# Kernel optimization log

Measured on AMD Instinct MI355X. Metric: run time of the kernel, lower is better.

Reference implementation:

```python
import jax, jax.numpy as jnp
import numpy as np

DIM = 768
NUM_HEADS = 12
HEAD_DIM = DIM // NUM_HEADS
SCALE = HEAD_DIM ** -0.5


def setup_inputs() -> dict:
    key = jax.random.key(0)
    ks = jax.random.split(key, 5)
    B, N, C = 2, 2048, DIM
    x = jax.random.normal(ks[0], (B, N, C), dtype=jnp.float32)
    # Dense layers: kernel [in, out], bias [out]
    w_qkv = jax.random.normal(ks[1], (C, 3 * C), dtype=jnp.float32) * (1.0 / np.sqrt(C))
    b_qkv = jnp.zeros((3 * C,), dtype=jnp.float32)
    w_proj = jax.random.normal(ks[2], (C, C), dtype=jnp.float32) * (1.0 / np.sqrt(C))
    b_proj = jnp.zeros((C,), dtype=jnp.float32)
    return {"x": x, "w_qkv": w_qkv, "b_qkv": b_qkv, "w_proj": w_proj, "b_proj": b_proj}


def reference(x, w_qkv, b_qkv, w_proj, b_proj):
    B, N, C = x.shape
    H, D = NUM_HEADS, HEAD_DIM
    qkv = x @ w_qkv + b_qkv                      # [B, N, 3C]
    qkv = qkv.reshape(B, N, 3, H, D).transpose(2, 0, 3, 1, 4)  # [3, B, H, N, D]
    q, k, v = qkv[0], qkv[1], qkv[2]
    # NOTE: original code applies scale AFTER q@k^T (scales scores), same math
    attn = jnp.einsum("bhnd,bhmd->bhnm", q, k) * SCALE  # [B, H, N, N]
    attn = jax.nn.softmax(attn, axis=-1)
    out = jnp.einsum("bhnm,bhmd->bhnd", attn, v)        # [B, H, N, D]
    out = out.transpose(0, 2, 1, 3).reshape(B, N, C)
    return out @ w_proj + b_proj
```

## Files before the change

kernel.cpp:

```cpp
#include <hip/hip_runtime.h>
#include <stdint.h>

typedef unsigned short u16;

typedef __bf16 bf16x8_ __attribute__((ext_vector_type(8)));
typedef float f32x4 __attribute__((ext_vector_type(4)));
typedef float f32x4__ __attribute__((ext_vector_type(4)));
typedef unsigned int u32x4_ __attribute__((ext_vector_type(4)));
typedef unsigned int u32x2_ __attribute__((ext_vector_type(2)));

typedef bf16x8_ __attribute__((may_alias)) bf16x8;
typedef u32x4_ __attribute__((may_alias)) u32x4;
typedef u32x2_ __attribute__((may_alias)) u32x2;
typedef f32x4__ __attribute__((may_alias)) f32x4a;

#define MFMA16(a, b, c) __builtin_amdgcn_mfma_f32_16x16x32_bf16(a, b, c, 0, 0, 0)
#define EXP2(x) __builtin_amdgcn_exp2f(x)

#define BN 2048
#define CDIM 768
#define HEADS 12
#define HD 64
#define NBH 24
#define MROWS 4096
#define QSC 0.1803368801111244f
#define SMAX 16.0f

__device__ __forceinline__ u16 f2bf(float f) {
    __bf16 h = (__bf16)f;
    return __builtin_bit_cast(u16, h);
}

__device__ __forceinline__ void gload_lds16(const void* g, void* l) {
    auto* gp = reinterpret_cast<const __attribute__((address_space(1))) unsigned int*>(
        reinterpret_cast<uintptr_t>(g));
    auto* lp = reinterpret_cast<__attribute__((address_space(3))) unsigned int*>(
        reinterpret_cast<uintptr_t>(l));
    __builtin_amdgcn_global_load_lds(gp, lp, 16, 0, 0);
}

__global__ void cast_x_kernel(const float* __restrict__ in, u16* __restrict__ out, int n8) {
    int i = blockIdx.x * 256 + threadIdx.x;
    if (i >= n8) return;
    const f32x4a* p = (const f32x4a*)in;
    f32x4a a = p[2 * (size_t)i], b = p[2 * (size_t)i + 1];
    union { u16 h[8]; u32x4_ v; } o;
#pragma unroll
    for (int j = 0; j < 4; ++j) { o.h[j] = f2bf(a[j]); o.h[4 + j] = f2bf(b[j]); }
    *(u32x4*)(out + (size_t)8 * i) = o.v;
}

__global__ void transpose_to_bf16(const float* __restrict__ in, u16* __restrict__ out,
                                  int R, int C) {
    __shared__ u16 tile[64][66];
    int r0 = blockIdx.y * 64, c0 = blockIdx.x * 64;
    int tid = threadIdx.x;
#pragma unroll
    for (int i = 0; i < 16; ++i) {
        int idx = tid + i * 256;
        int r = idx >> 6, c = idx & 63;
        tile[r][c] = f2bf(in[(size_t)(r0 + r) * C + c0 + c]);
    }
    __syncthreads();
#pragma unroll
    for (int i = 0; i < 16; ++i) {
        int idx = tid + i * 256;
        int c = idx >> 6, r = idx & 63;
        out[(size_t)(c0 + c) * R + r0 + r] = tile[r][c];
    }
}

__global__ void transpose_v(const u16* __restrict__ in, u16* __restrict__ out) {
    __shared__ u16 tile[64][66];
    int bh = blockIdx.z, r0 = blockIdx.y * 64;
    const u16* pin = in + (size_t)bh * BN * HD;
    u16* pout = out + (size_t)bh * HD * BN;
    int tid = threadIdx.x;
#pragma unroll
    for (int i = 0; i < 2; ++i) {
        int idx = tid + i * 256;
        int r = idx >> 3, ch = idx & 7;
        u32x4 v = *(const u32x4*)(pin + (size_t)(r0 + r) * HD + ch * 8);
        *(u32x4*)(&tile[r][ch * 8]) = v;
    }
    __syncthreads();
#pragma unroll
    for (int i = 0; i < 16; ++i) {
        int idx = tid + i * 256;
        int c = idx >> 6, r = idx & 63;
        pout[(size_t)c * BN + r0 + r] = tile[r][c];
    }
}

template <int EPI>
__global__ __launch_bounds__(256) void gemm_bt(
    const u16* __restrict__ A, const u16* __restrict__ Bt,
    const float* __restrict__ bias, int M, int N, int K,
    u16* __restrict__ Qb, u16* __restrict__ Kb, u16* __restrict__ Vb,
    float* __restrict__ Out) {
    __shared__ u16 As[2][128 * 64];
    __shared__ u16 Bs[2][128 * 64];
    int tid = threadIdx.x;
    int wid = tid >> 6, lane = tid & 63, lr = lane & 15, lhi = lane >> 4;
    int wr = wid >> 1, wc = wid & 1;
    int m0 = blockIdx.x * 128, n0 = blockIdx.y * 128;

    int rsub = lane >> 3;
    int csw = ((lane & 7) ^ rsub) * 8;

    auto stage = [&](int b, int k0) {
#pragma unroll
        for (int it = 0; it < 4; ++it) {
            int grp = it * 4 + wid;
            int row = grp * 8 + rsub;
            gload_lds16(A + (size_t)(m0 + row) * K + k0 + csw, &As[b][grp * 512]);
            gload_lds16(Bt + (size_t)(n0 + row) * K + k0 + csw, &Bs[b][grp * 512]);
        }
    };

    f32x4 acc[4][4];
#pragma unroll
    for (int i = 0; i < 4; ++i)
#pragma unroll
        for (int j = 0; j < 4; ++j) acc[i][j] = f32x4{0.f, 0.f, 0.f, 0.f};

    stage(0, 0);
    __syncthreads();
    int cur = 0;

    for (int k0 = 0; k0 < K; k0 += 64) {
        if (k0 + 64 < K) stage(cur ^ 1, k0 + 64);

        const u16* Ac = As[cur];
        const u16* Bc = Bs[cur];
        bf16x8 af[2][4], bfr[2][4];
#pragma unroll
        for (int x = 0; x < 4; ++x) {
            int ra = wr * 64 + x * 16 + lr;
            af[0][x] = *(const bf16x8*)(Ac + ra * 64 + ((lhi ^ (ra & 7)) * 8));
            af[1][x] = *(const bf16x8*)(Ac + ra * 64 + (((4 + lhi) ^ (ra & 7)) * 8));
            int rb = wc * 64 + x * 16 + lr;
            bfr[0][x] = *(const bf16x8*)(Bc + rb * 64 + ((lhi ^ (rb & 7)) * 8));
            bfr[1][x] = *(const bf16x8*)(Bc + rb * 64 + (((4 + lhi) ^ (rb & 7)) * 8));
        }
#pragma unroll
        for (int kc = 0; kc < 2; ++kc)
#pragma unroll
            for (int mi = 0; mi < 4; ++mi)
#pragma unroll
                for (int ni = 0; ni < 4; ++ni)
                    acc[mi][ni] = MFMA16(af[kc][mi], bfr[kc][ni], acc[mi][ni]);

        __syncthreads();
        cur ^= 1;
    }

#pragma unroll
    for (int mi = 0; mi < 4; ++mi) {
#pragma unroll
        for (int ni = 0; ni < 4; ++ni) {
            int col = n0 + wc * 64 + ni * 16 + lr;
            float bv = bias[col];
#pragma unroll
            for (int j = 0; j < 4; ++j) {
                int row = m0 + wr * 64 + mi * 16 + lhi * 4 + j;
                float v = acc[mi][ni][j] + bv;
                if constexpr (EPI == 0) {
                    int three = (col >= 1536) ? 2 : (col >= 768 ? 1 : 0);
                    int rem = col - three * 768;
                    int h = rem >> 6, d = rem & 63;
                    int b = row >> 11, nn = row & 2047;
                    size_t dst = ((size_t)(b * HEADS + h) * BN + nn) * HD + d;
                    if (three == 0)      Qb[dst] = f2bf(v * QSC);
                    else if (three == 1) Kb[dst] = f2bf(v);
                    else                 Vb[dst] = f2bf(v);
                } else {
                    Out[(size_t)row * N + col] = v;
                }
            }
        }
    }
}

__global__ __launch_bounds__(256) void attn_kernel(
    const u16* __restrict__ Qb, const u16* __restrict__ Kb,
    const u16* __restrict__ Vt, u16* __restrict__ Ao) {
    __shared__ u16 Ks[2][64 * 64];
    __shared__ u16 Vs[2][64 * 64];
    __shared__ u16 Ps[4][16 * 64];
    int tid = threadIdx.x, wid = tid >> 6, lane = tid & 63, lr = lane & 15, lhi = lane >> 4;
    int bh = blockIdx.y;
    int q0 = blockIdx.x * 64;

    const u16* Kbase = Kb + (size_t)bh * BN * HD;
    const u16* Vbase = Vt + (size_t)bh * HD * BN;
    int srow = lane >> 3;
    int csw = ((lane & 7) ^ srow) * 8;

    auto stageKV = [&](int b, int tn) {
#pragma unroll
        for (int it = 0; it < 2; ++it) {
            int r0 = it * 32 + wid * 8;
            gload_lds16(Kbase + (size_t)(tn + r0 + srow) * HD + csw, &Ks[b][r0 * 64]);
            gload_lds16(Vbase + (size_t)(r0 + srow) * BN + tn + csw, &Vs[b][r0 * 64]);
        }
    };

    const u16* Qrow = Qb + ((size_t)bh * BN + q0 + wid * 16 + lr) * HD;
    bf16x8 qf0 = *(const bf16x8*)(Qrow + lhi * 8);
    bf16x8 qf1 = *(const bf16x8*)(Qrow + 32 + lhi * 8);

    f32x4 po[4];
#pragma unroll
    for (int i = 0; i < 4; ++i) po[i] = f32x4{0.f, 0.f, 0.f, 0.f};
    float lrun = 0.f;
    u16* Pw = Ps[wid];

    stageKV(0, 0);
    __syncthreads();
    int cur = 0;

    for (int t = 0; t < BN; t += 64) {
        if (t + 64 < BN) stageKV(cur ^ 1, t + 64);

        const u16* Kc = Ks[cur];
        const u16* Vc = Vs[cur];

        f32x4 st[4];
        __builtin_amdgcn_s_setprio(1);
#pragma unroll
        for (int kg = 0; kg < 4; ++kg) {
            int r = kg * 16 + lr;
            bf16x8 kf0 = *(const bf16x8*)(Kc + r * 64 + ((lhi ^ (r & 7)) * 8));
            bf16x8 kf1 = *(const bf16x8*)(Kc + r * 64 + (((4 + lhi) ^ (r & 7)) * 8));
            f32x4 z = f32x4{0.f, 0.f, 0.f, 0.f};
            z = MFMA16(kf0, qf0, z);
            st[kg] = MFMA16(kf1, qf1, z);
        }
        __builtin_amdgcn_s_setprio(0);

        float p[4][4];
        float ssum = 0.f;
#pragma unroll
        for (int kg = 0; kg < 4; ++kg)
#pragma unroll
            for (int j = 0; j < 4; ++j) {
                float e = EXP2(st[kg][j] - SMAX);
                p[kg][j] = e;
                ssum += e;
            }
        lrun += ssum;

#pragma unroll
        for (int kg = 0; kg < 4; ++kg) {
            union { u16 h[4]; u32x2_ v; } pk;
            pk.h[0] = f2bf(p[kg][0]); pk.h[1] = f2bf(p[kg][1]);
            pk.h[2] = f2bf(p[kg][2]); pk.h[3] = f2bf(p[kg][3]);
            int elem = lr * 64 + ((kg * 16 + lhi * 4) ^ ((lr & 7) * 8));
            *(u32x2*)(Pw + elem) = pk.v;
        }
        bf16x8 pa0 = *(const bf16x8*)(Pw + lr * 64 + ((lhi * 8) ^ ((lr & 7) * 8)));
        bf16x8 pa1 = *(const bf16x8*)(Pw + lr * 64 + ((32 + lhi * 8) ^ ((lr & 7) * 8)));

        __builtin_amdgcn_s_setprio(1);
#pragma unroll
        for (int dc = 0; dc < 4; ++dc) {
            int vr = dc * 16 + lr;
            bf16x8 v0 = *(const bf16x8*)(Vc + vr * 64 + ((lhi ^ (vr & 7)) * 8));
            bf16x8 v1 = *(const bf16x8*)(Vc + vr * 64 + (((4 + lhi) ^ (vr & 7)) * 8));
            po[dc] = MFMA16(pa0, v0, po[dc]);
            po[dc] = MFMA16(pa1, v1, po[dc]);
        }
        __builtin_amdgcn_s_setprio(0);

        __syncthreads();
        cur ^= 1;
    }

    lrun += __shfl_xor(lrun, 16);
    lrun += __shfl_xor(lrun, 32);

    int b = bh / HEADS, h = bh % HEADS;
    float linv[4];
#pragma unroll
    for (int j = 0; j < 4; ++j) linv[j] = 1.f / __shfl(lrun, lhi * 4 + j);
#pragma unroll
    for (int dc = 0; dc < 4; ++dc)
#pragma unroll
        for (int j = 0; j < 4; ++j) {
            int row = q0 + wid * 16 + lhi * 4 + j;
            size_t dst = ((size_t)(b * BN + row)) * CDIM + h * HD + dc * 16 + lr;
            Ao[dst] = f2bf(po[dc][j] * linv[j]);
        }
}

extern "C" void kernel_launch(void* const* d_in, const int* in_sizes, int n_in,
                              void* d_out, int out_size, void* d_ws, size_t ws_size,
                              hipStream_t stream) {
    const float* x      = (const float*)d_in[0];
    const float* w_qkv  = (const float*)d_in[1];
    const float* b_qkv  = (const float*)d_in[2];
    const float* w_proj = (const float*)d_in[3];
    const float* b_proj = (const float*)d_in[4];
    float* out = (float*)d_out;

    char* ws = (char*)d_ws;
    const size_t SZ_XBF   = (size_t)MROWS * CDIM * 2;
    const size_t SZ_WQKV  = (size_t)3 * CDIM * CDIM * 2;
    const size_t SZ_WPROJ = (size_t)CDIM * CDIM * 2;
    const size_t SZ_HEADS = (size_t)NBH * BN * HD * 2;

    u16* x_bf    = (u16*)ws; ws += SZ_XBF;
    u16* wqkv_t  = (u16*)ws; ws += SZ_WQKV;
    u16* wproj_t = (u16*)ws; ws += SZ_WPROJ;
    u16* Qb      = (u16*)ws; ws += SZ_HEADS;
    u16* Kb      = (u16*)ws; ws += SZ_HEADS;
    u16* Vb      = (u16*)ws; ws += SZ_HEADS;
    u16* Vt      = (u16*)ws; ws += SZ_HEADS;
    u16* Ao      = (u16*)ws; ws += SZ_XBF;

    cast_x_kernel<<<(MROWS * CDIM / 8 + 255) / 256, 256, 0, stream>>>(x, x_bf, MROWS * CDIM / 8);
    transpose_to_bf16<<<dim3(3 * CDIM / 64, CDIM / 64), 256, 0, stream>>>(w_qkv, wqkv_t, CDIM, 3 * CDIM);
    transpose_to_bf16<<<dim3(CDIM / 64, CDIM / 64), 256, 0, stream>>>(w_proj, wproj_t, CDIM, CDIM);
    gemm_bt<0><<<dim3(MROWS / 128, 3 * CDIM / 128), 256, 0, stream>>>(
        x_bf, wqkv_t, b_qkv, MROWS, 3 * CDIM, CDIM, Qb, Kb, Vb, nullptr);
    transpose_v<<<dim3(1, BN / 64, NBH), 256, 0, stream>>>(Vb, Vt);
    attn_kernel<<<dim3(BN / 64, NBH), 256, 0, stream>>>(Qb, Kb, Vt, Ao);
    gemm_bt<1><<<dim3(MROWS / 128, CDIM / 128), 256, 0, stream>>>(
        Ao, wproj_t, b_proj, MROWS, CDIM, CDIM, nullptr, nullptr, nullptr, out);
}
```

Baseline: 168.8 us.

## Fuse prep kernels, write V transposed in QKV GEMM epilogue, swizzle block order

Merges the x cast and both weight transposes into one prep launch. The QKV GEMM epilogue now stages V blocks through shared memory and writes them directly in transposed layout, which removes the separate transpose_v kernel and the intermediate V buffer. GEMM and attention grids become 1D with an XCD-aware block swizzle that groups neighbouring tiles for cache locality. These changes cut launch overhead and memory traffic, at the cost of an extra LDS round trip and a barrier in the V epilogue.

```diff
diff --git a/kernel.cpp b/kernel.cpp
--- a/kernel.cpp
+++ b/kernel.cpp
@@ -2,6 +2,7 @@
 #include <stdint.h>
 
 typedef unsigned short u16;
+typedef unsigned int u32;
 
 typedef __bf16 bf16x8_ __attribute__((ext_vector_type(8)));
 typedef float f32x4 __attribute__((ext_vector_type(4)));
@@ -12,6 +13,7 @@
 typedef bf16x8_ __attribute__((may_alias)) bf16x8;
 typedef u32x4_ __attribute__((may_alias)) u32x4;
 typedef u32x2_ __attribute__((may_alias)) u32x2;
+typedef u32 __attribute__((may_alias)) u32a;
 typedef f32x4__ __attribute__((may_alias)) f32x4a;
 
 #define MFMA16(a, b, c) __builtin_amdgcn_mfma_f32_16x16x32_bf16(a, b, c, 0, 0, 0)
@@ -30,6 +32,11 @@
     __bf16 h = (__bf16)f;
     return __builtin_bit_cast(u16, h);
 }
+__device__ __forceinline__ u32 pkbf(float lo, float hi) {
+    union { u16 h[2]; u32 w; } u;
+    u.h[0] = f2bf(lo); u.h[1] = f2bf(hi);
+    return u.w;
+}
 
 __device__ __forceinline__ void gload_lds16(const void* g, void* l) {
     auto* gp = reinterpret_cast<const __attribute__((address_space(1))) unsigned int*>(
@@ -39,22 +46,26 @@
     __builtin_amdgcn_global_load_lds(gp, lp, 16, 0, 0);
 }
 
-__global__ void cast_x_kernel(const float* __restrict__ in, u16* __restrict__ out, int n8) {
-    int i = blockIdx.x * 256 + threadIdx.x;
-    if (i >= n8) return;
-    const f32x4a* p = (const f32x4a*)in;
-    f32x4a a = p[2 * (size_t)i], b = p[2 * (size_t)i + 1];
-    union { u16 h[8]; u32x4_ v; } o;
-#pragma unroll
-    for (int j = 0; j < 4; ++j) { o.h[j] = f2bf(a[j]); o.h[4 + j] = f2bf(b[j]); }
-    *(u32x4*)(out + (size_t)8 * i) = o.v;
-}
-
-__global__ void transpose_to_bf16(const float* __restrict__ in, u16* __restrict__ out,
-                                  int R, int C) {
+__global__ __launch_bounds__(256) void prep_kernel(
+    const float* __restrict__ x, u16* __restrict__ x_bf,
+    const float* __restrict__ w_qkv, u16* __restrict__ wqkv_t,
+    const float* __restrict__ w_proj, u16* __restrict__ wproj_t) {
     __shared__ u16 tile[64][66];
-    int r0 = blockIdx.y * 64, c0 = blockIdx.x * 64;
-    int tid = threadIdx.x;
+    int bid = blockIdx.x, tid = threadIdx.x;
+    if (bid < 1536) {
+        size_t i = (size_t)bid * 256 + tid;
+        const f32x4a* p = (const f32x4a*)x;
+        f32x4a a = p[2 * i], b = p[2 * i + 1];
+        union { u16 h[8]; u32x4_ v; } o;
+#pragma unroll
+        for (int j = 0; j < 4; ++j) { o.h[j] = f2bf(a[j]); o.h[4 + j] = f2bf(b[j]); }
+        *(u32x4*)(x_bf + 8 * i) = o.v;
+        return;
+    }
+    const float* in; u16* out; int C, bx, by;
+    if (bid < 1968) { in = w_qkv;  out = wqkv_t;  C = 3 * CDIM; bx = (bid - 1536) % 36; by = (bid - 1536) / 36; }
+    else            { in = w_proj; out = wproj_t; C = CDIM;     bx = (bid - 1968) % 12; by = (bid - 1968) / 12; }
+    int r0 = by * 64, c0 = bx * 64;
 #pragma unroll
     for (int i = 0; i < 16; ++i) {
         int idx = tid + i * 256;
@@ -66,55 +77,39 @@
     for (int i = 0; i < 16; ++i) {
         int idx = tid + i * 256;
         int c = idx >> 6, r = idx & 63;
-        out[(size_t)(c0 + c) * R + r0 + r] = tile[r][c];
-    }
-}
-
-__global__ void transpose_v(const u16* __restrict__ in, u16* __restrict__ out) {
-    __shared__ u16 tile[64][66];
-    int bh = blockIdx.z, r0 = blockIdx.y * 64;
-    const u16* pin = in + (size_t)bh * BN * HD;
-    u16* pout = out + (size_t)bh * HD * BN;
-    int tid = threadIdx.x;
-#pragma unroll
-    for (int i = 0; i < 2; ++i) {
-        int idx = tid + i * 256;
-        int r = idx >> 3, ch = idx & 7;
-        u32x4 v = *(const u32x4*)(pin + (size_t)(r0 + r) * HD + ch * 8);
-        *(u32x4*)(&tile[r][ch * 8]) = v;
-    }
-    __syncthreads();
-#pragma unroll
-    for (int i = 0; i < 16; ++i) {
-        int idx = tid + i * 256;
-        int c = idx >> 6, r = idx & 63;
-        pout[(size_t)c * BN + r0 + r] = tile[r][c];
+        out[(size_t)(c0 + c) * CDIM + r0 + r] = tile[r][c];
     }
 }
 
 template <int EPI>
 __global__ __launch_bounds__(256) void gemm_bt(
     const u16* __restrict__ A, const u16* __restrict__ Bt,
-    const float* __restrict__ bias, int M, int N, int K,
-    u16* __restrict__ Qb, u16* __restrict__ Kb, u16* __restrict__ Vb,
+    const float* __restrict__ bias, int N, int K,
+    u16* __restrict__ Qb, u16* __restrict__ Kb, u16* __restrict__ Vt,
     float* __restrict__ Out) {
-    __shared__ u16 As[2][128 * 64];
-    __shared__ u16 Bs[2][128 * 64];
+    __shared__ u16 sh[32768];
     int tid = threadIdx.x;
     int wid = tid >> 6, lane = tid & 63, lr = lane & 15, lhi = lane >> 4;
     int wr = wid >> 1, wc = wid & 1;
-    int m0 = blockIdx.x * 128, n0 = blockIdx.y * 128;
+
+    int nwg = gridDim.x, cpx = nwg >> 3;
+    int bid = blockIdx.x;
+    int swz = (bid & 7) * cpx + (bid >> 3);
+    int m0 = (swz & 31) * 128;
+    int n0 = (swz >> 5) * 128;
 
     int rsub = lane >> 3;
     int csw = ((lane & 7) ^ rsub) * 8;
 
     auto stage = [&](int b, int k0) {
+        u16* As = sh + b * 8192;
+        u16* Bs = sh + 16384 + b * 8192;
 #pragma unroll
         for (int it = 0; it < 4; ++it) {
             int grp = it * 4 + wid;
             int row = grp * 8 + rsub;
-            gload_lds16(A + (size_t)(m0 + row) * K + k0 + csw, &As[b][grp * 512]);
-            gload_lds16(Bt + (size_t)(n0 + row) * K + k0 + csw, &Bs[b][grp * 512]);
+            gload_lds16(A + (size_t)(m0 + row) * K + k0 + csw, As + grp * 512);
+            gload_lds16(Bt + (size_t)(n0 + row) * K + k0 + csw, Bs + grp * 512);
         }
     };
 
@@ -131,8 +126,8 @@
     for (int k0 = 0; k0 < K; k0 += 64) {
         if (k0 + 64 < K) stage(cur ^ 1, k0 + 64);
 
-        const u16* Ac = As[cur];
-        const u16* Bc = Bs[cur];
+        const u16* Ac = sh + cur * 8192;
+        const u16* Bc = sh + 16384 + cur * 8192;
         bf16x8 af[2][4], bfr[2][4];
 #pragma unroll
         for (int x = 0; x < 4; ++x) {
@@ -155,30 +150,65 @@
         cur ^= 1;
     }
 
-#pragma unroll
-    for (int mi = 0; mi < 4; ++mi) {
-#pragma unroll
-        for (int ni = 0; ni < 4; ++ni) {
-            int col = n0 + wc * 64 + ni * 16 + lr;
-            float bv = bias[col];
-#pragma unroll
-            for (int j = 0; j < 4; ++j) {
-                int row = m0 + wr * 64 + mi * 16 + lhi * 4 + j;
-                float v = acc[mi][ni][j] + bv;
-                if constexpr (EPI == 0) {
-                    int three = (col >= 1536) ? 2 : (col >= 768 ? 1 : 0);
-                    int rem = col - three * 768;
+    if constexpr (EPI == 0) {
+        if (n0 >= 1536) {
+            u16* tileT = sh;
+#pragma unroll
+            for (int mi = 0; mi < 4; ++mi)
+#pragma unroll
+                for (int ni = 0; ni < 4; ++ni) {
+                    int c = wc * 64 + ni * 16 + lr;
+                    float bv = bias[n0 + c];
+                    int r = wr * 64 + mi * 16 + lhi * 4;
+                    *(u32a*)(tileT + c * 136 + r)     = pkbf(acc[mi][ni][0] + bv, acc[mi][ni][1] + bv);
+                    *(u32a*)(tileT + c * 136 + r + 2) = pkbf(acc[mi][ni][2] + bv, acc[mi][ni][3] + bv);
+                }
+            __syncthreads();
+            int h0 = (n0 - 1536) >> 6;
+            int b = m0 >> 11;
+            int nbase = m0 & 2047;
+#pragma unroll
+            for (int it = 0; it < 8; ++it) {
+                int idx = tid + it * 256;
+                int c = idx >> 4, r0 = (idx & 15) * 8;
+                u32x4 v = *(const u32x4*)(tileT + c * 136 + r0);
+                int bh = b * HEADS + h0 + (c >> 6), d = c & 63;
+                *(u32x4*)(Vt + ((size_t)bh * HD + d) * BN + nbase + r0) = v;
+            }
+        } else {
+#pragma unroll
+            for (int mi = 0; mi < 4; ++mi)
+#pragma unroll
+                for (int ni = 0; ni < 4; ++ni) {
+                    int col = n0 + wc * 64 + ni * 16 + lr;
+                    float bv = bias[col];
+                    int isK = col >= 768;
+                    int rem = col - (isK ? 768 : 0);
                     int h = rem >> 6, d = rem & 63;
-                    int b = row >> 11, nn = row & 2047;
-                    size_t dst = ((size_t)(b * HEADS + h) * BN + nn) * HD + d;
-                    if (three == 0)      Qb[dst] = f2bf(v * QSC);
-                    else if (three == 1) Kb[dst] = f2bf(v);
-                    else                 Vb[dst] = f2bf(v);
-                } else {
-                    Out[(size_t)row * N + col] = v;
+#pragma unroll
+                    for (int j = 0; j < 4; ++j) {
+                        int row = m0 + wr * 64 + mi * 16 + lhi * 4 + j;
+                        float v = acc[mi][ni][j] + bv;
+                        int b = row >> 11, nn = row & 2047;
+                        size_t dst = ((size_t)(b * HEADS + h) * BN + nn) * HD + d;
+                        if (isK) Kb[dst] = f2bf(v);
+                        else     Qb[dst] = f2bf(v * QSC);
+                    }
+                }
+        }
+    } else {
+#pragma unroll
+        for (int mi = 0; mi < 4; ++mi)
+#pragma unroll
+            for (int ni = 0; ni < 4; ++ni) {
+                int col = n0 + wc * 64 + ni * 16 + lr;
+                float bv = bias[col];
+#pragma unroll
+                for (int j = 0; j < 4; ++j) {
+                    int row = m0 + wr * 64 + mi * 16 + lhi * 4 + j;
+                    Out[(size_t)row * N + col] = acc[mi][ni][j] + bv;
                 }
             }
-        }
     }
 }
 
@@ -189,8 +219,10 @@
     __shared__ u16 Vs[2][64 * 64];
     __shared__ u16 Ps[4][16 * 64];
     int tid = threadIdx.x, wid = tid >> 6, lane = tid & 63, lr = lane & 15, lhi = lane >> 4;
-    int bh = blockIdx.y;
-    int q0 = blockIdx.x * 64;
+    int bid = blockIdx.x;
+    int swz = (bid & 7) * 96 + (bid >> 3);
+    int bh = swz >> 5;
+    int q0 = (swz & 31) * 64;
 
     const u16* Kbase = Kb + (size_t)bh * BN * HD;
     const u16* Vbase = Vt + (size_t)bh * HD * BN;
@@ -253,11 +285,11 @@
 
 #pragma unroll
         for (int kg = 0; kg < 4; ++kg) {
-            union { u16 h[4]; u32x2_ v; } pk;
-            pk.h[0] = f2bf(p[kg][0]); pk.h[1] = f2bf(p[kg][1]);
-            pk.h[2] = f2bf(p[kg][2]); pk.h[3] = f2bf(p[kg][3]);
+            u32x2_ pk;
+            pk[0] = pkbf(p[kg][0], p[kg][1]);
+            pk[1] = pkbf(p[kg][2], p[kg][3]);
             int elem = lr * 64 + ((kg * 16 + lhi * 4) ^ ((lr & 7) * 8));
-            *(u32x2*)(Pw + elem) = pk.v;
+            *(u32x2*)(Pw + elem) = pk;
         }
         bf16x8 pa0 = *(const bf16x8*)(Pw + lr * 64 + ((lhi * 8) ^ ((lr & 7) * 8)));
         bf16x8 pa1 = *(const bf16x8*)(Pw + lr * 64 + ((32 + lhi * 8) ^ ((lr & 7) * 8)));
@@ -315,17 +347,13 @@
     u16* wproj_t = (u16*)ws; ws += SZ_WPROJ;
     u16* Qb      = (u16*)ws; ws += SZ_HEADS;
     u16* Kb      = (u16*)ws; ws += SZ_HEADS;
-    u16* Vb      = (u16*)ws; ws += SZ_HEADS;
     u16* Vt      = (u16*)ws; ws += SZ_HEADS;
     u16* Ao      = (u16*)ws; ws += SZ_XBF;
 
-    cast_x_kernel<<<(MROWS * CDIM / 8 + 255) / 256, 256, 0, stream>>>(x, x_bf, MROWS * CDIM / 8);
-    transpose_to_bf16<<<dim3(3 * CDIM / 64, CDIM / 64), 256, 0, stream>>>(w_qkv, wqkv_t, CDIM, 3 * CDIM);
-    transpose_to_bf16<<<dim3(CDIM / 64, CDIM / 64), 256, 0, stream>>>(w_proj, wproj_t, CDIM, CDIM);
-    gemm_bt<0><<<dim3(MROWS / 128, 3 * CDIM / 128), 256, 0, stream>>>(
-        x_bf, wqkv_t, b_qkv, MROWS, 3 * CDIM, CDIM, Qb, Kb, Vb, nullptr);
-    transpose_v<<<dim3(1, BN / 64, NBH), 256, 0, stream>>>(Vb, Vt);
-    attn_kernel<<<dim3(BN / 64, NBH), 256, 0, stream>>>(Qb, Kb, Vt, Ao);
-    gemm_bt<1><<<dim3(MROWS / 128, CDIM / 128), 256, 0, stream>>>(
-        Ao, wproj_t, b_proj, MROWS, CDIM, CDIM, nullptr, nullptr, nullptr, out);
-}
+    prep_kernel<<<2112, 256, 0, stream>>>(x, x_bf, w_qkv, wqkv_t, w_proj, wproj_t);
+    gemm_bt<0><<<576, 256, 0, stream>>>(
+        x_bf, wqkv_t, b_qkv, 3 * CDIM, CDIM, Qb, Kb, Vt, nullptr);
+    attn_kernel<<<768, 256, 0, stream>>>(Qb, Kb, Vt, Ao);
+    gemm_bt<1><<<192, 256, 0, stream>>>(
+        Ao, wproj_t, b_proj, CDIM, CDIM, nullptr, nullptr, nullptr, out);
+}
```

New measurement: 160.8 us. -4.7%, faster.
